# Performance work log

Measured on AMD Instinct MI355X. Metric: run time of the kernel, lower is better.

Reference implementation:

```python
import jax, jax.numpy as jnp
import numpy as np
import math

B, S, D = 8, 1024, 512      # batch, seq_len, d_model
H = 8                       # n_heads
DK = D                      # per-head dim forced to d_model by the view() quirk
EPS = 1e-6


def setup_inputs() -> dict:
    key = jax.random.key(0)
    ks = jax.random.split(key, 8)
    # xavier_uniform for (out, in) = (H*DK, D)
    lim_qkv = math.sqrt(6.0 / (H * DK + D))
    lim_fc = math.sqrt(6.0 / (D + H * DK))
    return {
        "q": jax.random.normal(ks[0], (B, S, D), jnp.float32),
        "k": jax.random.normal(ks[1], (B, S, D), jnp.float32),
        "v": jax.random.normal(ks[2], (B, S, D), jnp.float32),
        "w_q": jax.random.uniform(ks[3], (H * DK, D), jnp.float32, -lim_qkv, lim_qkv),
        "w_k": jax.random.uniform(ks[4], (H * DK, D), jnp.float32, -lim_qkv, lim_qkv),
        "w_v": jax.random.uniform(ks[5], (H * DK, D), jnp.float32, -lim_qkv, lim_qkv),
        "w_fc": jax.random.uniform(ks[6], (D, H * DK), jnp.float32, -lim_fc, lim_fc),
        "gamma": jnp.ones((D,), jnp.float32),
        "beta": jnp.zeros((D,), jnp.float32),
    }


def reference(q, k, v, w_q, w_k, w_v, w_fc, gamma, beta):
    residual = q
    # project then view as (B, S, H, d_q) with d_q = d_model (source's quirk)
    qh = (q @ w_q.T).reshape(B, S, H, DK).transpose(0, 2, 1, 3)  # (B,H,S,DK)
    kh = (k @ w_k.T).reshape(B, S, H, DK).transpose(0, 2, 1, 3)
    vh = (v @ w_v.T).reshape(B, S, H, DK).transpose(0, 2, 1, 3)
    # scaled dot-product attention; scale by sqrt(d_q) = sqrt(d_model)
    scale = 1.0 / math.sqrt(DK)
    attn = jnp.einsum("bhqd,bhkd->bhqk", qh, kh) * scale  # (B,H,S,S)
    attn = jax.nn.softmax(attn, axis=-1)
    out = jnp.einsum("bhqk,bhkd->bhqd", attn, vh)          # (B,H,S,DK)
    out = out.transpose(0, 2, 1, 3).reshape(B, S, H * DK)  # (B,S,H*DK)
    out = out @ w_fc.T                                      # (B,S,D); dropout = identity (eval)
    out = out + residual
    # LayerNorm(eps=1e-6)
    mu = jnp.mean(out, axis=-1, keepdims=True)
    var = jnp.var(out, axis=-1, keepdims=True)
    out = (out - mu) * jax.lax.rsqrt(var + EPS) * gamma + beta
    return out
```

## Files before the change

kernel.cpp:

```cpp
#include <hip/hip_runtime.h>
#include <hip/hip_bf16.h>
#include <stdint.h>

typedef __attribute__((ext_vector_type(8))) short short8;
typedef __attribute__((ext_vector_type(4))) float f32x4;

__device__ __forceinline__ short f2bf(float f) {
  __hip_bfloat16 h = __float2bfloat16(f);
  union { __hip_bfloat16 h; short s; } x;
  x.h = h;
  return x.s;
}
__device__ __forceinline__ void g2lds16(const void* g, void* l) {
  __builtin_amdgcn_global_load_lds(
      (const __attribute__((address_space(1))) void*)g,
      (__attribute__((address_space(3))) void*)l, 16, 0, 0);
}

__global__ void cvt6(const float* __restrict__ q, const float* __restrict__ k,
                     const float* __restrict__ v, const float* __restrict__ wq,
                     const float* __restrict__ wk, const float* __restrict__ wv,
                     short* __restrict__ xb, short* __restrict__ wb)
{
  const int z = blockIdx.z;
  const float* s;
  short* d;
  long nvec;
  if (z < 3) { s = (z == 0) ? q : (z == 1) ? k : v;  d = xb + (long)z * 4194304; nvec = 524288; }
  else       { s = (z == 3) ? wq : (z == 4) ? wk : wv; d = wb + (long)(z - 3) * 2097152; nvec = 262144; }
  const long stride = (long)gridDim.x * blockDim.x;
  for (long i = (long)blockIdx.x * blockDim.x + threadIdx.x; i < nvec; i += stride) {
    f32x4 a = *(const f32x4*)(s + i * 8);
    f32x4 b = *(const f32x4*)(s + i * 8 + 4);
    short8 o;
#pragma unroll
    for (int t = 0; t < 4; ++t) { o[t] = f2bf(a[t]); o[4 + t] = f2bf(b[t]); }
    *(short8*)(d + i * 8) = o;
  }
}

__global__ void cvt1(const float* __restrict__ s, short* __restrict__ d, int nvec)
{
  const long stride = (long)gridDim.x * blockDim.x;
  for (long i = (long)blockIdx.x * blockDim.x + threadIdx.x; i < nvec; i += stride) {
    f32x4 a = *(const f32x4*)(s + i * 8);
    f32x4 b = *(const f32x4*)(s + i * 8 + 4);
    short8 o;
#pragma unroll
    for (int t = 0; t < 4; ++t) { o[t] = f2bf(a[t]); o[4 + t] = f2bf(b[t]); }
    *(short8*)(d + i * 8) = o;
  }
}

__global__ void qkv_proj(
    const short* __restrict__ xb, const short* __restrict__ wb,
    short* __restrict__ Qh, short* __restrict__ Kh, short* __restrict__ Vt)
{
  __shared__ __align__(16) short As[2][128 * 32];
  __shared__ __align__(16) short Bs[2][128 * 32];
  const int z = blockIdx.z;
  const short* x = xb + (long)z * 4194304;
  const short* W = wb + (long)z * 2097152;
  short* out = (z == 0) ? Qh : (z == 1) ? Kh : Vt;
  const int tid = threadIdx.x;
  const int wave = tid >> 6, lane = tid & 63;
  const int quad = lane >> 4, l15 = lane & 15;
  const int mBase = blockIdx.x * 128, nBase = blockIdx.y * 128;
  const int wm = wave >> 1, wn = wave & 1;
  const int c0 = tid, c1 = tid + 256;
  const int r0 = c0 >> 2, o0 = (c0 & 3) * 8;
  const int r1 = c1 >> 2, o1 = (c1 & 3) * 8;
  f32x4 acc[4][4] = {};

  auto stage = [&](int kk, int b_) {
    g2lds16(x + (long)(mBase + r0) * 512 + kk + o0, (char*)(As[b_]) + c0 * 16);
    g2lds16(x + (long)(mBase + r1) * 512 + kk + o1, (char*)(As[b_]) + c1 * 16);
    g2lds16(W + (long)(nBase + r0) * 512 + kk + o0, (char*)(Bs[b_]) + c0 * 16);
    g2lds16(W + (long)(nBase + r1) * 512 + kk + o1, (char*)(Bs[b_]) + c1 * 16);
  };
  stage(0, 0);

  for (int it = 0; it < 16; ++it) {
    const int buf = it & 1;
    stage(((it + 1) & 15) * 32, buf ^ 1);
    __builtin_amdgcn_sched_barrier(0);
    asm volatile("s_waitcnt vmcnt(4)" ::: "memory");
    __builtin_amdgcn_s_barrier();
    __builtin_amdgcn_sched_barrier(0);
    short8 a[4], b[4];
#pragma unroll
    for (int mi = 0; mi < 4; ++mi)
      a[mi] = *(const short8*)(As[buf] + (wm * 64 + mi * 16 + l15) * 32 + quad * 8);
#pragma unroll
    for (int ni = 0; ni < 4; ++ni)
      b[ni] = *(const short8*)(Bs[buf] + (wn * 64 + ni * 16 + l15) * 32 + quad * 8);
#pragma unroll
    for (int mi = 0; mi < 4; ++mi)
#pragma unroll
      for (int ni = 0; ni < 4; ++ni)
        acc[mi][ni] = __builtin_amdgcn_mfma_f32_16x16x32_bf16(a[mi], b[ni], acc[mi][ni], 0, 0, 0);
    __builtin_amdgcn_s_barrier();
    __builtin_amdgcn_sched_barrier(0);
  }
  asm volatile("s_waitcnt vmcnt(0)" ::: "memory");

#pragma unroll
  for (int mi = 0; mi < 4; ++mi) {
#pragma unroll
    for (int ni = 0; ni < 4; ++ni) {
      int n = nBase + wn * 64 + ni * 16 + l15;
      int h = n >> 9, d = n & 511;
#pragma unroll
      for (int r = 0; r < 4; ++r) {
        int m = mBase + wm * 64 + mi * 16 + quad * 4 + r;
        int b = m >> 10, s = m & 1023;
        long idx;
        if (z == 2) idx = ((long)(b * 8 + h) * 512 + d) * 1024 + s;
        else        idx = ((long)(b * 8 + h) * 1024 + s) * 512 + d;
        out[idx] = f2bf(acc[mi][ni][r]);
      }
    }
  }
}

__global__ __launch_bounds__(512, 2) void flash_attn(
    const short* __restrict__ Qh, const short* __restrict__ Kh,
    const short* __restrict__ Vt, short* __restrict__ ctx)
{
  __shared__ __align__(16) short Ks[2][32 * 512];
  __shared__ __align__(16) short Vs[512 * 32];
  __shared__ __align__(16) short Ps[8 * 16 * 40];
  __shared__ float lred[128];
  const int tid = threadIdx.x;
  const int wave = tid >> 6, lane = tid & 63;
  const int quad = lane >> 4, l15 = lane & 15;
  const int lin = blockIdx.x;
  const int qt = (lin >> 3) & 7;
  const int bh = ((lin >> 6) << 3) | (lin & 7);
  const float C = 0.0637587234f;

  const short* qbase = Qh + ((long)bh * 1024 + qt * 128 + wave * 16 + l15) * 512 + quad * 8;
  short8 qf[16];
#pragma unroll
  for (int c = 0; c < 16; ++c) qf[c] = *(const short8*)(qbase + c * 32);

  auto stageK = [&](int kt_, int b_) {
#pragma unroll
    for (int i = 0; i < 4; ++i) {
      int c = i * 512 + tid;
      int r = c >> 6, j = (c & 63) ^ (r & 7);
      g2lds16(Kh + ((long)bh * 1024 + kt_ * 32 + r) * 512 + j * 8, (char*)(Ks[b_]) + c * 16);
    }
  };
  auto stageV = [&](int kt_) {
#pragma unroll
    for (int i = 0; i < 4; ++i) {
      int c = i * 512 + tid;
      int d = c >> 2, j = (c & 3) ^ (d & 3);
      g2lds16(Vt + ((long)bh * 512 + d) * 1024 + kt_ * 32 + j * 8, (char*)Vs + c * 16);
    }
  };
  stageK(0, 0);

  f32x4 acc[8][4] = {};
  float l[4] = {0.f, 0.f, 0.f, 0.f};

  for (int kt = 0; kt < 32; ++kt) {
    const int buf = kt & 1;
    stageK((kt + 1) & 31, buf ^ 1);
    __builtin_amdgcn_sched_barrier(0);
    stageV(kt);
    __builtin_amdgcn_sched_barrier(0);
    asm volatile("s_waitcnt vmcnt(8)" ::: "memory");
    __builtin_amdgcn_s_barrier();
    __builtin_amdgcn_sched_barrier(0);

    const short* ks = Ks[buf];
    f32x4 sacc[2] = {};
#pragma unroll
    for (int nt = 0; nt < 2; ++nt)
#pragma unroll
      for (int c = 0; c < 16; ++c) {
        int row = nt * 16 + l15;
        int j = (c * 4 + quad) ^ (row & 7);
        short8 kf = *(const short8*)(ks + row * 512 + j * 8);
        sacc[nt] = __builtin_amdgcn_mfma_f32_16x16x32_bf16(qf[c], kf, sacc[nt], 0, 0, 0);
      }
#pragma unroll
    for (int r = 0; r < 4; ++r) {
      float p0 = exp2f(sacc[0][r] * C);
      float p1 = exp2f(sacc[1][r] * C);
      Ps[wave * 640 + (quad * 4 + r) * 40 + l15]      = f2bf(p0);
      Ps[wave * 640 + (quad * 4 + r) * 40 + 16 + l15] = f2bf(p1);
      l[r] += p0 + p1;
    }
    asm volatile("s_waitcnt vmcnt(4) lgkmcnt(0)" ::: "memory");
    __builtin_amdgcn_s_barrier();
    __builtin_amdgcn_sched_barrier(0);

    short8 vf[4];
#pragma unroll
    for (int t = 0; t < 4; ++t) {
      int row = wave * 64 + t * 16 + l15;
      int j = quad ^ (row & 3);
      vf[t] = *(const short8*)(Vs + row * 32 + j * 8);
    }
#pragma unroll
    for (int g = 0; g < 8; ++g) {
      short8 pf = *(const short8*)(Ps + g * 640 + l15 * 40 + quad * 8);
#pragma unroll
      for (int t = 0; t < 4; ++t)
        acc[g][t] = __builtin_amdgcn_mfma_f32_16x16x32_bf16(pf, vf[t], acc[g][t], 0, 0, 0);
    }
    asm volatile("s_waitcnt lgkmcnt(0)" ::: "memory");
    __builtin_amdgcn_s_barrier();
    __builtin_amdgcn_sched_barrier(0);
  }
#pragma unroll
  for (int r = 0; r < 4; ++r) {
    float t = l[r];
    t += __shfl_xor(t, 1);
    t += __shfl_xor(t, 2);
    t += __shfl_xor(t, 4);
    t += __shfl_xor(t, 8);
    l[r] = t;
  }
  if (l15 == 0) {
#pragma unroll
    for (int r = 0; r < 4; ++r) lred[wave * 16 + quad * 4 + r] = l[r];
  }
  __syncthreads();
  const int b = bh >> 3, h = bh & 7;
#pragma unroll
  for (int g = 0; g < 8; ++g) {
#pragma unroll
    for (int r = 0; r < 4; ++r) {
      float inv = 1.0f / lred[g * 16 + quad * 4 + r];
      int qrow = qt * 128 + g * 16 + quad * 4 + r;
      long base = ((long)(b * 1024 + qrow)) * 4096 + h * 512 + wave * 64;
#pragma unroll
      for (int t = 0; t < 4; ++t)
        ctx[base + t * 16 + l15] = f2bf(acc[g][t][r] * inv);
    }
  }
}

__global__ void fc_gemm(
    const short* __restrict__ A, const short* __restrict__ Wb,
    const float* __restrict__ resid, float* __restrict__ Y)
{
  __shared__ __align__(16) short As[2][128 * 32];
  __shared__ __align__(16) short Bs[2][64 * 32];
  const int tid = threadIdx.x;
  const int wave = tid >> 6, lane = tid & 63;
  const int quad = lane >> 4, l15 = lane & 15;
  const int mBase = blockIdx.x * 128, nBase = blockIdx.y * 64;
  const int wm = wave >> 1, wn = wave & 1;
  const int c0 = tid, c1 = tid + 256;
  const int r0 = c0 >> 2, o0 = (c0 & 3) * 8;
  const int r1 = c1 >> 2, o1 = (c1 & 3) * 8;
  f32x4 acc[4][2] = {};

  auto stage = [&](int kk, int b_) {
    g2lds16(A + (long)(mBase + r0) * 4096 + kk + o0, (char*)(As[b_]) + c0 * 16);
    g2lds16(A + (long)(mBase + r1) * 4096 + kk + o1, (char*)(As[b_]) + c1 * 16);
    g2lds16(Wb + (long)(nBase + r0) * 4096 + kk + o0, (char*)(Bs[b_]) + c0 * 16);
  };
  stage(0, 0);

  for (int it = 0; it < 128; ++it) {
    const int buf = it & 1;
    stage(((it + 1) & 127) * 32, buf ^ 1);
    __builtin_amdgcn_sched_barrier(0);
    asm volatile("s_waitcnt vmcnt(3)" ::: "memory");
    __builtin_amdgcn_s_barrier();
    __builtin_amdgcn_sched_barrier(0);
    short8 a[4], b[2];
#pragma unroll
    for (int mi = 0; mi < 4; ++mi)
      a[mi] = *(const short8*)(As[buf] + (wm * 64 + mi * 16 + l15) * 32 + quad * 8);
#pragma unroll
    for (int ni = 0; ni < 2; ++ni)
      b[ni] = *(const short8*)(Bs[buf] + (wn * 32 + ni * 16 + l15) * 32 + quad * 8);
#pragma unroll
    for (int mi = 0; mi < 4; ++mi)
#pragma unroll
      for (int ni = 0; ni < 2; ++ni)
        acc[mi][ni] = __builtin_amdgcn_mfma_f32_16x16x32_bf16(a[mi], b[ni], acc[mi][ni], 0, 0, 0);
    __builtin_amdgcn_s_barrier();
    __builtin_amdgcn_sched_barrier(0);
  }
  asm volatile("s_waitcnt vmcnt(0)" ::: "memory");

#pragma unroll
  for (int mi = 0; mi < 4; ++mi)
#pragma unroll
    for (int ni = 0; ni < 2; ++ni) {
      int n = nBase + wn * 32 + ni * 16 + l15;
#pragma unroll
      for (int r = 0; r < 4; ++r) {
        int m = mBase + wm * 64 + mi * 16 + quad * 4 + r;
        long idx = (long)m * 512 + n;
        Y[idx] = acc[mi][ni][r] + resid[idx];
      }
    }
}

__global__ void layernorm(
    const float* __restrict__ Y, const float* __restrict__ gamma,
    const float* __restrict__ beta, float* __restrict__ out)
{
  const int tid = threadIdx.x;
  const int wave = tid >> 6, lane = tid & 63;
  const long row = (long)blockIdx.x * 4 + wave;
  f32x4 xa = *(const f32x4*)(Y + row * 512 + lane * 8);
  f32x4 xb = *(const f32x4*)(Y + row * 512 + lane * 8 + 4);
  float x[8];
  float s = 0.f, s2 = 0.f;
#pragma unroll
  for (int i = 0; i < 4; ++i) { x[i] = xa[i]; x[i + 4] = xb[i]; }
#pragma unroll
  for (int i = 0; i < 8; ++i) { s += x[i]; s2 += x[i] * x[i]; }
#pragma unroll
  for (int m = 1; m < 64; m <<= 1) { s += __shfl_xor(s, m); s2 += __shfl_xor(s2, m); }
  float mu = s * (1.0f / 512.0f);
  float var = s2 * (1.0f / 512.0f) - mu * mu;
  float rs = rsqrtf(var + 1e-6f);
  f32x4 oa, ob;
#pragma unroll
  for (int i = 0; i < 4; ++i) {
    oa[i] = (x[i] - mu) * rs * gamma[lane * 8 + i] + beta[lane * 8 + i];
    ob[i] = (x[i + 4] - mu) * rs * gamma[lane * 8 + 4 + i] + beta[lane * 8 + 4 + i];
  }
  *(f32x4*)(out + row * 512 + lane * 8) = oa;
  *(f32x4*)(out + row * 512 + lane * 8 + 4) = ob;
}

extern "C" void kernel_launch(void* const* d_in, const int* in_sizes, int n_in,
                              void* d_out, int out_size, void* d_ws, size_t ws_size,
                              hipStream_t stream) {
  const float* q     = (const float*)d_in[0];
  const float* k     = (const float*)d_in[1];
  const float* v     = (const float*)d_in[2];
  const float* wq    = (const float*)d_in[3];
  const float* wk    = (const float*)d_in[4];
  const float* wv    = (const float*)d_in[5];
  const float* wfc   = (const float*)d_in[6];
  const float* gamma = (const float*)d_in[7];
  const float* beta  = (const float*)d_in[8];
  float* out = (float*)d_out;
  char* ws = (char*)d_ws;
  short* Qh  = (short*)(ws);
  short* Kh  = (short*)(ws + 67108864);
  short* Vt  = (short*)(ws + 134217728);
  short* ctx = (short*)(ws + 201326592);
  short* xb  = (short*)(ws + 201326592);
  short* wb  = xb + 3 * 4194304;
  short* wfcb = (short*)(ws + 16777216);
  float* Y   = (float*)(ws);

  cvt6<<<dim3(1024, 1, 6), 256, 0, stream>>>(q, k, v, wq, wk, wv, xb, wb);
  qkv_proj<<<dim3(64, 32, 3), 256, 0, stream>>>(xb, wb, Qh, Kh, Vt);
  flash_attn<<<dim3(512), 512, 0, stream>>>(Qh, Kh, Vt, ctx);
  cvt1<<<dim3(1024), 256, 0, stream>>>(wfc, wfcb, 262144);
  fc_gemm<<<dim3(64, 8), 256, 0, stream>>>(ctx, wfcb, q, Y);
  layernorm<<<2048, 256, 0, stream>>>(Y, gamma, beta, out);
}
```

Baseline: 655.2 us.

## Deepen GEMM K-tiles to 64 and double-buffer V in flash attention

The QKV and FC GEMMs now stage 64-wide K slices, which halves the loop trip count and the number of barriers per tile. Each iteration waits for the current buffer before issuing the prefetch, so one barrier per iteration is enough. In flash attention, V is now double-buffered and prefetched one step ahead together with K, which removes the trailing barrier. s_setprio is raised around the MFMA loops, and launch bounds drop to one block per CU to fit the larger LDS footprint. This risks lower occupancy in attention, and the 64-element-wide LDS rows are not swizzled, which may cause bank conflicts.

```diff
diff --git a/kernel.cpp b/kernel.cpp
--- a/kernel.cpp
+++ b/kernel.cpp
@@ -56,8 +56,8 @@
     const short* __restrict__ xb, const short* __restrict__ wb,
     short* __restrict__ Qh, short* __restrict__ Kh, short* __restrict__ Vt)
 {
-  __shared__ __align__(16) short As[2][128 * 32];
-  __shared__ __align__(16) short Bs[2][128 * 32];
+  __shared__ __align__(16) short As[2][128 * 64];
+  __shared__ __align__(16) short Bs[2][128 * 64];
   const int z = blockIdx.z;
   const short* x = xb + (long)z * 4194304;
   const short* W = wb + (long)z * 2097152;
@@ -67,40 +67,46 @@
   const int quad = lane >> 4, l15 = lane & 15;
   const int mBase = blockIdx.x * 128, nBase = blockIdx.y * 128;
   const int wm = wave >> 1, wn = wave & 1;
-  const int c0 = tid, c1 = tid + 256;
-  const int r0 = c0 >> 2, o0 = (c0 & 3) * 8;
-  const int r1 = c1 >> 2, o1 = (c1 & 3) * 8;
   f32x4 acc[4][4] = {};
 
   auto stage = [&](int kk, int b_) {
-    g2lds16(x + (long)(mBase + r0) * 512 + kk + o0, (char*)(As[b_]) + c0 * 16);
-    g2lds16(x + (long)(mBase + r1) * 512 + kk + o1, (char*)(As[b_]) + c1 * 16);
-    g2lds16(W + (long)(nBase + r0) * 512 + kk + o0, (char*)(Bs[b_]) + c0 * 16);
-    g2lds16(W + (long)(nBase + r1) * 512 + kk + o1, (char*)(Bs[b_]) + c1 * 16);
+#pragma unroll
+    for (int i = 0; i < 4; ++i) {
+      int c = i * 256 + tid;
+      int r = c >> 3, o = (c & 7) * 8;
+      g2lds16(x + (long)(mBase + r) * 512 + kk + o, (char*)(As[b_]) + c * 16);
+    }
+#pragma unroll
+    for (int i = 0; i < 4; ++i) {
+      int c = i * 256 + tid;
+      int r = c >> 3, o = (c & 7) * 8;
+      g2lds16(W + (long)(nBase + r) * 512 + kk + o, (char*)(Bs[b_]) + c * 16);
+    }
   };
   stage(0, 0);
 
-  for (int it = 0; it < 16; ++it) {
+  for (int it = 0; it < 8; ++it) {
     const int buf = it & 1;
-    stage(((it + 1) & 15) * 32, buf ^ 1);
-    __builtin_amdgcn_sched_barrier(0);
-    asm volatile("s_waitcnt vmcnt(4)" ::: "memory");
+    asm volatile("s_waitcnt vmcnt(0)" ::: "memory");
     __builtin_amdgcn_s_barrier();
     __builtin_amdgcn_sched_barrier(0);
-    short8 a[4], b[4];
-#pragma unroll
-    for (int mi = 0; mi < 4; ++mi)
-      a[mi] = *(const short8*)(As[buf] + (wm * 64 + mi * 16 + l15) * 32 + quad * 8);
-#pragma unroll
-    for (int ni = 0; ni < 4; ++ni)
-      b[ni] = *(const short8*)(Bs[buf] + (wn * 64 + ni * 16 + l15) * 32 + quad * 8);
-#pragma unroll
-    for (int mi = 0; mi < 4; ++mi)
+    stage(((it + 1) & 7) * 64, buf ^ 1);
+    __builtin_amdgcn_sched_barrier(0);
+#pragma unroll
+    for (int kk = 0; kk < 2; ++kk) {
+      short8 a[4], b[4];
+#pragma unroll
+      for (int mi = 0; mi < 4; ++mi)
+        a[mi] = *(const short8*)(As[buf] + (wm * 64 + mi * 16 + l15) * 64 + kk * 32 + quad * 8);
 #pragma unroll
       for (int ni = 0; ni < 4; ++ni)
-        acc[mi][ni] = __builtin_amdgcn_mfma_f32_16x16x32_bf16(a[mi], b[ni], acc[mi][ni], 0, 0, 0);
-    __builtin_amdgcn_s_barrier();
-    __builtin_amdgcn_sched_barrier(0);
+        b[ni] = *(const short8*)(Bs[buf] + (wn * 64 + ni * 16 + l15) * 64 + kk * 32 + quad * 8);
+#pragma unroll
+      for (int mi = 0; mi < 4; ++mi)
+#pragma unroll
+        for (int ni = 0; ni < 4; ++ni)
+          acc[mi][ni] = __builtin_amdgcn_mfma_f32_16x16x32_bf16(a[mi], b[ni], acc[mi][ni], 0, 0, 0);
+    }
   }
   asm volatile("s_waitcnt vmcnt(0)" ::: "memory");
 
@@ -123,12 +129,12 @@
   }
 }
 
-__global__ __launch_bounds__(512, 2) void flash_attn(
+__global__ __launch_bounds__(512, 1) void flash_attn(
     const short* __restrict__ Qh, const short* __restrict__ Kh,
     const short* __restrict__ Vt, short* __restrict__ ctx)
 {
   __shared__ __align__(16) short Ks[2][32 * 512];
-  __shared__ __align__(16) short Vs[512 * 32];
+  __shared__ __align__(16) short Vs[2][512 * 32];
   __shared__ __align__(16) short Ps[8 * 16 * 40];
   __shared__ float lred[128];
   const int tid = threadIdx.x;
@@ -152,31 +158,32 @@
       g2lds16(Kh + ((long)bh * 1024 + kt_ * 32 + r) * 512 + j * 8, (char*)(Ks[b_]) + c * 16);
     }
   };
-  auto stageV = [&](int kt_) {
+  auto stageV = [&](int kt_, int b_) {
 #pragma unroll
     for (int i = 0; i < 4; ++i) {
       int c = i * 512 + tid;
       int d = c >> 2, j = (c & 3) ^ (d & 3);
-      g2lds16(Vt + ((long)bh * 512 + d) * 1024 + kt_ * 32 + j * 8, (char*)Vs + c * 16);
+      g2lds16(Vt + ((long)bh * 512 + d) * 1024 + kt_ * 32 + j * 8, (char*)(Vs[b_]) + c * 16);
     }
   };
   stageK(0, 0);
+  stageV(0, 0);
 
   f32x4 acc[8][4] = {};
   float l[4] = {0.f, 0.f, 0.f, 0.f};
 
   for (int kt = 0; kt < 32; ++kt) {
     const int buf = kt & 1;
+    asm volatile("s_waitcnt vmcnt(4)" ::: "memory");
+    __builtin_amdgcn_s_barrier();
+    __builtin_amdgcn_sched_barrier(0);
     stageK((kt + 1) & 31, buf ^ 1);
-    __builtin_amdgcn_sched_barrier(0);
-    stageV(kt);
-    __builtin_amdgcn_sched_barrier(0);
-    asm volatile("s_waitcnt vmcnt(8)" ::: "memory");
-    __builtin_amdgcn_s_barrier();
+    stageV((kt + 1) & 31, buf ^ 1);
     __builtin_amdgcn_sched_barrier(0);
 
     const short* ks = Ks[buf];
     f32x4 sacc[2] = {};
+    __builtin_amdgcn_s_setprio(1);
 #pragma unroll
     for (int nt = 0; nt < 2; ++nt)
 #pragma unroll
@@ -186,6 +193,7 @@
         short8 kf = *(const short8*)(ks + row * 512 + j * 8);
         sacc[nt] = __builtin_amdgcn_mfma_f32_16x16x32_bf16(qf[c], kf, sacc[nt], 0, 0, 0);
       }
+    __builtin_amdgcn_s_setprio(0);
 #pragma unroll
     for (int r = 0; r < 4; ++r) {
       float p0 = exp2f(sacc[0][r] * C);
@@ -194,17 +202,19 @@
       Ps[wave * 640 + (quad * 4 + r) * 40 + 16 + l15] = f2bf(p1);
       l[r] += p0 + p1;
     }
-    asm volatile("s_waitcnt vmcnt(4) lgkmcnt(0)" ::: "memory");
+    asm volatile("s_waitcnt vmcnt(8) lgkmcnt(0)" ::: "memory");
     __builtin_amdgcn_s_barrier();
     __builtin_amdgcn_sched_barrier(0);
 
+    const short* vs = Vs[buf];
     short8 vf[4];
 #pragma unroll
     for (int t = 0; t < 4; ++t) {
       int row = wave * 64 + t * 16 + l15;
       int j = quad ^ (row & 3);
-      vf[t] = *(const short8*)(Vs + row * 32 + j * 8);
-    }
+      vf[t] = *(const short8*)(vs + row * 32 + j * 8);
+    }
+    __builtin_amdgcn_s_setprio(1);
 #pragma unroll
     for (int g = 0; g < 8; ++g) {
       short8 pf = *(const short8*)(Ps + g * 640 + l15 * 40 + quad * 8);
@@ -212,9 +222,7 @@
       for (int t = 0; t < 4; ++t)
         acc[g][t] = __builtin_amdgcn_mfma_f32_16x16x32_bf16(pf, vf[t], acc[g][t], 0, 0, 0);
     }
-    asm volatile("s_waitcnt lgkmcnt(0)" ::: "memory");
-    __builtin_amdgcn_s_barrier();
-    __builtin_amdgcn_sched_barrier(0);
+    __builtin_amdgcn_s_setprio(0);
   }
 #pragma unroll
   for (int r = 0; r < 4; ++r) {
@@ -249,46 +257,53 @@
     const short* __restrict__ A, const short* __restrict__ Wb,
     const float* __restrict__ resid, float* __restrict__ Y)
 {
-  __shared__ __align__(16) short As[2][128 * 32];
-  __shared__ __align__(16) short Bs[2][64 * 32];
+  __shared__ __align__(16) short As[2][128 * 64];
+  __shared__ __align__(16) short Bs[2][64 * 64];
   const int tid = threadIdx.x;
   const int wave = tid >> 6, lane = tid & 63;
   const int quad = lane >> 4, l15 = lane & 15;
   const int mBase = blockIdx.x * 128, nBase = blockIdx.y * 64;
   const int wm = wave >> 1, wn = wave & 1;
-  const int c0 = tid, c1 = tid + 256;
-  const int r0 = c0 >> 2, o0 = (c0 & 3) * 8;
-  const int r1 = c1 >> 2, o1 = (c1 & 3) * 8;
   f32x4 acc[4][2] = {};
 
   auto stage = [&](int kk, int b_) {
-    g2lds16(A + (long)(mBase + r0) * 4096 + kk + o0, (char*)(As[b_]) + c0 * 16);
-    g2lds16(A + (long)(mBase + r1) * 4096 + kk + o1, (char*)(As[b_]) + c1 * 16);
-    g2lds16(Wb + (long)(nBase + r0) * 4096 + kk + o0, (char*)(Bs[b_]) + c0 * 16);
+#pragma unroll
+    for (int i = 0; i < 4; ++i) {
+      int c = i * 256 + tid;
+      int r = c >> 3, o = (c & 7) * 8;
+      g2lds16(A + (long)(mBase + r) * 4096 + kk + o, (char*)(As[b_]) + c * 16);
+    }
+#pragma unroll
+    for (int i = 0; i < 2; ++i) {
+      int c = i * 256 + tid;
+      int r = c >> 3, o = (c & 7) * 8;
+      g2lds16(Wb + (long)(nBase + r) * 4096 + kk + o, (char*)(Bs[b_]) + c * 16);
+    }
   };
   stage(0, 0);
 
-  for (int it = 0; it < 128; ++it) {
+  for (int it = 0; it < 64; ++it) {
     const int buf = it & 1;
-    stage(((it + 1) & 127) * 32, buf ^ 1);
-    __builtin_amdgcn_sched_barrier(0);
-    asm volatile("s_waitcnt vmcnt(3)" ::: "memory");
+    asm volatile("s_waitcnt vmcnt(0)" ::: "memory");
     __builtin_amdgcn_s_barrier();
     __builtin_amdgcn_sched_barrier(0);
-    short8 a[4], b[2];
-#pragma unroll
-    for (int mi = 0; mi < 4; ++mi)
-      a[mi] = *(const short8*)(As[buf] + (wm * 64 + mi * 16 + l15) * 32 + quad * 8);
-#pragma unroll
-    for (int ni = 0; ni < 2; ++ni)
-      b[ni] = *(const short8*)(Bs[buf] + (wn * 32 + ni * 16 + l15) * 32 + quad * 8);
-#pragma unroll
-    for (int mi = 0; mi < 4; ++mi)
+    stage(((it + 1) & 63) * 64, buf ^ 1);
+    __builtin_amdgcn_sched_barrier(0);
+#pragma unroll
+    for (int kk = 0; kk < 2; ++kk) {
+      short8 a[4], b[2];
+#pragma unroll
+      for (int mi = 0; mi < 4; ++mi)
+        a[mi] = *(const short8*)(As[buf] + (wm * 64 + mi * 16 + l15) * 64 + kk * 32 + quad * 8);
 #pragma unroll
       for (int ni = 0; ni < 2; ++ni)
-        acc[mi][ni] = __builtin_amdgcn_mfma_f32_16x16x32_bf16(a[mi], b[ni], acc[mi][ni], 0, 0, 0);
-    __builtin_amdgcn_s_barrier();
-    __builtin_amdgcn_sched_barrier(0);
+        b[ni] = *(const short8*)(Bs[buf] + (wn * 32 + ni * 16 + l15) * 64 + kk * 32 + quad * 8);
+#pragma unroll
+      for (int mi = 0; mi < 4; ++mi)
+#pragma unroll
+        for (int ni = 0; ni < 2; ++ni)
+          acc[mi][ni] = __builtin_amdgcn_mfma_f32_16x16x32_bf16(a[mi], b[ni], acc[mi][ni], 0, 0, 0);
+    }
   }
   asm volatile("s_waitcnt vmcnt(0)" ::: "memory");
 
```

After: 702.4 us. +7.2%, slower.
